# Performance work log

Hardware: AMD Instinct MI355X
Metric: run time of the kernel (lower is better)

The kernel has to match this reference:

```python
import jax, jax.numpy as jnp
import numpy as np

NUM_HEADS = 16
HEAD_DIM = 64
ROPE_BASE = 160000.0


def _rope_tables(seq_len, head_dim):
    inv_freq = 1.0 / (ROPE_BASE ** (jnp.arange(0, head_dim, 2, dtype=jnp.float32) / head_dim))
    freqs = jnp.arange(seq_len, dtype=jnp.float32)[:, None] * inv_freq[None, :]  # [S, hd/2]
    return jnp.cos(freqs)[None, None], jnp.sin(freqs)[None, None]  # [1,1,S,hd/2]


def _apply_rope(x, cos, sin):
    # x: [B, nh, S, hd]; split-half rotation as in the torch module
    x1, x2 = jnp.split(x, 2, axis=-1)
    return jnp.concatenate([x1 * cos - x2 * sin, x2 * cos + x1 * sin], axis=-1)


def setup_inputs() -> dict:
    key = jax.random.key(0)
    k1, k2, k3 = jax.random.split(key, 3)
    B, S, H = 2, 2048, 1024
    hidden_states = jax.random.normal(k1, (B, S, H), dtype=jnp.float32)
    # additive causal mask: 0 for allowed, -1e9 for future positions
    causal = jnp.tril(jnp.ones((S, S), dtype=bool))
    attention_mask = jnp.where(causal, 0.0, -1e9).astype(jnp.float32)[None, None]
    Wqkv = jax.random.normal(k2, (H, 3 * H), dtype=jnp.float32) * (H ** -0.5)
    Wo = jax.random.normal(k3, (H, H), dtype=jnp.float32) * (H ** -0.5)
    return {"hidden_states": hidden_states, "attention_mask": attention_mask, "Wqkv": Wqkv, "Wo": Wo}


def reference(hidden_states, attention_mask, Wqkv, Wo):
    B, S, H = hidden_states.shape
    nh, hd = NUM_HEADS, HEAD_DIM
    scale = hd ** -0.5

    qkv = hidden_states @ Wqkv                                   # [B,S,3H]
    qkv = qkv.reshape(B, S, 3, nh, hd).transpose(2, 0, 3, 1, 4)  # [3,B,nh,S,hd]
    q, k, v = qkv[0], qkv[1], qkv[2]

    cos, sin = _rope_tables(S, hd)
    q = _apply_rope(q, cos, sin)
    k = _apply_rope(k, cos, sin)

    scores = jnp.einsum('bhqd,bhkd->bhqk', q, k) * scale + attention_mask
    attn = jax.nn.softmax(scores, axis=-1)
    out = jnp.einsum('bhqk,bhkd->bhqd', attn, v)                 # [B,nh,S,hd]
    out = out.transpose(0, 2, 1, 3).reshape(B, S, H)
    return out @ Wo
```

## Files before the change

### kernel.cpp

```cpp
#include <hip/hip_runtime.h>
#include <hip/hip_bf16.h>

typedef __bf16 bf16x8 __attribute__((ext_vector_type(8)));
typedef float f32x4 __attribute__((ext_vector_type(4)));
typedef unsigned short u16;

__device__ __forceinline__ u16 f2bf(float f) {
    union { float f; unsigned u; } x{f};
    unsigned r = x.u + 0x7fffu + ((x.u >> 16) & 1u);
    return (u16)(r >> 16);
}
__device__ __forceinline__ unsigned pk2(float a, float b) {
    union { float f; unsigned u; } x{a}, y{b};
    return ((x.u + 0x8000u) >> 16) | ((y.u + 0x8000u) & 0xffff0000u);
}
__device__ __forceinline__ float ex2(float x) { return __builtin_amdgcn_exp2f(x); }
__device__ __forceinline__ f32x4 zero4() { f32x4 z = {0.f, 0.f, 0.f, 0.f}; return z; }

typedef const __attribute__((address_space(1))) unsigned int* gp1_t;
typedef __attribute__((address_space(3))) unsigned int* lp3_t;
__device__ __forceinline__ void async16(const u16* g, u16* l) {
    __builtin_amdgcn_global_load_lds((gp1_t)g, (lp3_t)l, 16, 0, 0);
}

__global__ void __launch_bounds__(256) prep(const float* __restrict__ hs,
                                            u16* __restrict__ Xb,
                                            const float* __restrict__ Wqkv,
                                            u16* __restrict__ Wqkvt,
                                            const float* __restrict__ Wo,
                                            u16* __restrict__ Wot,
                                            float* __restrict__ cosT,
                                            float* __restrict__ sinT) {
    __shared__ float tile[32][33];
    const int blk = blockIdx.x, t = threadIdx.x;
    if (blk < 4096) {
        int i = (blk * 256 + t) * 4;
        float4 v = *(const float4*)(hs + i);
        ushort4 o;
        o.x = f2bf(v.x); o.y = f2bf(v.y); o.z = f2bf(v.z); o.w = f2bf(v.w);
        *(ushort4*)(Xb + i) = o;
    } else if (blk < 8192) {
        const float* W; u16* Wt; int N, bx, by;
        if (blk < 7168) { int bid = blk - 4096; W = Wqkv; Wt = Wqkvt; N = 3072; bx = bid % 96; by = bid / 96; }
        else            { int bid = blk - 7168; W = Wo;   Wt = Wot;   N = 1024; bx = bid % 32; by = bid / 32; }
        const int K = 1024;
        int tx = t & 31, ty = t >> 5;
        int n0 = bx * 32, k0 = by * 32;
#pragma unroll
        for (int i = 0; i < 32; i += 8)
            tile[ty + i][tx] = W[(size_t)(k0 + ty + i) * N + n0 + tx];
        __syncthreads();
#pragma unroll
        for (int i = 0; i < 32; i += 8)
            Wt[(size_t)(n0 + ty + i) * K + k0 + tx] = f2bf(tile[tx][ty + i]);
    } else {
        int idx = (blk - 8192) * 256 + t;
        int d = idx & 31, s = idx >> 5;
        float inv = expf(-(float)d * 0.374466538f);
        float th = (float)s * inv;
        cosT[idx] = cosf(th);
        sinT[idx] = sinf(th);
    }
}

struct GemmCtx {
    f32x4 acc[4][4];
    int m16, q4, wm, wn;
};
template <int KDIM>
__device__ __forceinline__ void gemm_loop(const u16* __restrict__ A,
                                          const u16* __restrict__ Bt,
                                          int bm, int bn, GemmCtx& cx,
                                          u16* As, u16* Bs) {
    const int t = threadIdx.x;
    const int lane = t & 63, w = t >> 6;
    cx.wm = w >> 1; cx.wn = w & 1;
    cx.m16 = lane & 15; cx.q4 = lane >> 4;

    const int lrow = lane >> 2;
    const int kchunk = (lane & 3) ^ ((lane >> 3) & 3);
    const u16* Ag = A + (size_t)(bm * 128 + w * 32 + lrow) * KDIM + kchunk * 8;
    const u16* Bg = Bt + (size_t)(bn * 128 + w * 32 + lrow) * KDIM + kchunk * 8;
    const int l0 = (w * 32) * 32;
    const int l1 = (w * 32 + 16) * 32;
    const int kswz = (cx.q4 ^ ((cx.m16 >> 1) & 3)) * 8;

#pragma unroll
    for (int i = 0; i < 4; i++)
#pragma unroll
        for (int j = 0; j < 4; j++) cx.acc[i][j] = zero4();

    constexpr int NT = KDIM / 32;
    async16(Ag, As + l0);
    async16(Ag + 16 * KDIM, As + l1);
    async16(Bg, Bs + l0);
    async16(Bg + 16 * KDIM, Bs + l1);
    async16(Ag + 32, As + 4096 + l0);
    async16(Ag + 16 * KDIM + 32, As + 4096 + l1);
    async16(Bg + 32, Bs + 4096 + l0);
    async16(Bg + 16 * KDIM + 32, Bs + 4096 + l1);

    int co = 0, po = 2 * 4096;
#pragma unroll 1
    for (int tt = 0; tt < NT; ++tt) {
        if (tt + 1 < NT) {
            asm volatile("s_waitcnt vmcnt(4)" ::: "memory");
        } else {
            asm volatile("s_waitcnt vmcnt(0)" ::: "memory");
        }
        __builtin_amdgcn_s_barrier();
        __builtin_amdgcn_sched_barrier(0);
        if (tt + 2 < NT) {
            const int k0 = (tt + 2) * 32;
            async16(Ag + k0, As + po + l0);
            async16(Ag + 16 * KDIM + k0, As + po + l1);
            async16(Bg + k0, Bs + po + l0);
            async16(Bg + 16 * KDIM + k0, Bs + po + l1);
        }
        __builtin_amdgcn_sched_barrier(0);

        bf16x8 af[4], bf[4];
#pragma unroll
        for (int i = 0; i < 4; i++)
            af[i] = *(const bf16x8*)&As[co + (cx.wm * 64 + i * 16 + cx.m16) * 32 + kswz];
#pragma unroll
        for (int j = 0; j < 4; j++)
            bf[j] = *(const bf16x8*)&Bs[co + (cx.wn * 64 + j * 16 + cx.m16) * 32 + kswz];
#pragma unroll
        for (int i = 0; i < 4; i++)
#pragma unroll
            for (int j = 0; j < 4; j++)
                cx.acc[i][j] = __builtin_amdgcn_mfma_f32_16x16x32_bf16(af[i], bf[j], cx.acc[i][j], 0, 0, 0);

        asm volatile("" ::: "memory");
        __builtin_amdgcn_sched_barrier(0);
        co += 4096; if (co == 12288) co = 0;
        po += 4096; if (po == 12288) po = 0;
    }
}

struct GemmCtx2 {
    f32x4 acc[4][8];
    int m16, q4, wm;
};
template <int KDIM>
__device__ __forceinline__ void gemm_loop2(const u16* __restrict__ A,
                                           const u16* __restrict__ Bt,
                                           int bm, int bn, GemmCtx2& cx,
                                           u16* As, u16* Bs) {
    const int t = threadIdx.x;
    const int lane = t & 63, w = t >> 6;
    cx.wm = w;
    cx.m16 = lane & 15; cx.q4 = lane >> 4;

    const int lrow = lane >> 2;
    const int kchunk = (lane & 3) ^ ((lane >> 3) & 3);
    const u16* Ag = A + (size_t)(bm * 128 + w * 64 + lrow) * KDIM + kchunk * 8;
    const u16* Bg = Bt + (size_t)(bn * 128 + w * 64 + lrow) * KDIM + kchunk * 8;
    const int lb = (w * 64) * 32;
    const int kswz = (cx.q4 ^ ((cx.m16 >> 1) & 3)) * 8;

#pragma unroll
    for (int i = 0; i < 4; i++)
#pragma unroll
        for (int j = 0; j < 8; j++) cx.acc[i][j] = zero4();

    constexpr int NT = KDIM / 32;
#pragma unroll
    for (int c = 0; c < 4; c++) {
        async16(Ag + c * 16 * KDIM, As + lb + c * 16 * 32);
        async16(Bg + c * 16 * KDIM, Bs + lb + c * 16 * 32);
    }
#pragma unroll
    for (int c = 0; c < 4; c++) {
        async16(Ag + 32 + c * 16 * KDIM, As + 4096 + lb + c * 16 * 32);
        async16(Bg + 32 + c * 16 * KDIM, Bs + 4096 + lb + c * 16 * 32);
    }

    int co = 0, po = 2 * 4096;
#pragma unroll 1
    for (int tt = 0; tt < NT; ++tt) {
        if (tt + 1 < NT) {
            asm volatile("s_waitcnt vmcnt(8)" ::: "memory");
        } else {
            asm volatile("s_waitcnt vmcnt(0)" ::: "memory");
        }
        __builtin_amdgcn_s_barrier();
        __builtin_amdgcn_sched_barrier(0);
        if (tt + 2 < NT) {
            const int k0 = (tt + 2) * 32;
#pragma unroll
            for (int c = 0; c < 4; c++) {
                async16(Ag + k0 + c * 16 * KDIM, As + po + lb + c * 16 * 32);
                async16(Bg + k0 + c * 16 * KDIM, Bs + po + lb + c * 16 * 32);
            }
        }
        __builtin_amdgcn_sched_barrier(0);

        bf16x8 af[4], bf[8];
#pragma unroll
        for (int i = 0; i < 4; i++)
            af[i] = *(const bf16x8*)&As[co + (cx.wm * 64 + i * 16 + cx.m16) * 32 + kswz];
#pragma unroll
        for (int j = 0; j < 8; j++)
            bf[j] = *(const bf16x8*)&Bs[co + (j * 16 + cx.m16) * 32 + kswz];
#pragma unroll
        for (int i = 0; i < 4; i++)
#pragma unroll
            for (int j = 0; j < 8; j++)
                cx.acc[i][j] = __builtin_amdgcn_mfma_f32_16x16x32_bf16(af[i], bf[j], cx.acc[i][j], 0, 0, 0);

        asm volatile("" ::: "memory");
        __builtin_amdgcn_sched_barrier(0);
        co += 4096; if (co == 12288) co = 0;
        po += 4096; if (po == 12288) po = 0;
    }
}

__global__ void __launch_bounds__(128, 2) gemm_qkv(const u16* __restrict__ A,
                                                   const u16* __restrict__ Bt,
                                                   const float* __restrict__ cosT,
                                                   const float* __restrict__ sinT,
                                                   u16* __restrict__ Q,
                                                   u16* __restrict__ Kd,
                                                   u16* __restrict__ Vt) {
    __shared__ __align__(16) u16 As[3 * 128 * 32];
    __shared__ __align__(16) u16 Bs[3 * 128 * 32];
    GemmCtx2 cx;
    const int hw = blockIdx.x;
    const int orig = (hw & 7) * 96 + (hw >> 3);
    const int bm = orig / 24, bn = orig % 24;
    gemm_loop2<1024>(A, Bt, bm, bn, cx, As, Bs);
    const int m16 = cx.m16, q4 = cx.q4;

    const int colblk = bn * 128;
    const int type = colblk >> 10;
    const int h0 = (colblk & 1023) >> 6;
    const int rbase = bm * 128 + cx.wm * 64;

    if (type == 2) {
#pragma unroll
        for (int i = 0; i < 4; i++) {
            int s0 = rbase + i * 16 + q4 * 4;
            int b = s0 >> 11, sl = s0 & 2047;
#pragma unroll
            for (int j = 0; j < 8; j++) {
                int h = h0 + (j >> 2);
                int d = (j & 3) * 16 + m16;
                size_t ob = (size_t)(b * 16 + h) * 64 * 2048;
                ushort4 o;
                o.x = f2bf(cx.acc[i][j][0]);
                o.y = f2bf(cx.acc[i][j][1]);
                o.z = f2bf(cx.acc[i][j][2]);
                o.w = f2bf(cx.acc[i][j][3]);
                *(ushort4*)&Vt[ob + (size_t)d * 2048 + sl] = o;
            }
        }
    } else {
        u16* dst = (type == 0) ? Q : Kd;
        const float qs = (type == 0) ? 0.1803368801f  : 1.0f;
#pragma unroll
        for (int i = 0; i < 4; i++)
#pragma unroll
            for (int rr = 0; rr < 4; rr++) {
                int r = rbase + i * 16 + q4 * 4 + rr;
                int b = r >> 11, s = r & 2047;
#pragma unroll
                for (int hh = 0; hh < 2; hh++) {
                    size_t ob = ((size_t)((b * 16 + h0 + hh) * 2048 + s)) * 64;
#pragma unroll
                    for (int j2 = 0; j2 < 2; j2++) {
                        int d = j2 * 16 + m16;
                        float cs = cosT[s * 32 + d];
                        float sn = sinT[s * 32 + d];
                        float x1 = cx.acc[i][hh * 4 + j2][rr];
                        float x2 = cx.acc[i][hh * 4 + j2 + 2][rr];
                        dst[ob + d]      = f2bf((x1 * cs - x2 * sn) * qs);
                        dst[ob + d + 32] = f2bf((x2 * cs + x1 * sn) * qs);
                    }
                }
            }
    }
}

__global__ void __launch_bounds__(256) gemm_out(const u16* __restrict__ A,
                                                const u16* __restrict__ Bt,
                                                float* __restrict__ C) {
    __shared__ __align__(16) u16 As[3 * 128 * 32];
    __shared__ __align__(16) u16 Bs[3 * 128 * 32];
    GemmCtx cx;
    const int bm = blockIdx.y, bn = blockIdx.x;
    gemm_loop<1024>(A, Bt, bm, bn, cx, As, Bs);
    const int N = 1024;
#pragma unroll
    for (int i = 0; i < 4; i++)
#pragma unroll
        for (int j = 0; j < 4; j++)
#pragma unroll
            for (int rr = 0; rr < 4; rr++) {
                int row = bm * 128 + cx.wm * 64 + i * 16 + cx.q4 * 4 + rr;
                int col = bn * 128 + cx.wn * 64 + j * 16 + cx.m16;
                C[(size_t)row * N + col] = cx.acc[i][j][rr];
            }
}

__global__ void __launch_bounds__(512) attn_kernel(const u16* __restrict__ Q,
                                                   const u16* __restrict__ Kg_,
                                                   const u16* __restrict__ Vtg_,
                                                   u16* __restrict__ O) {
    __shared__ __align__(16) u16 Ks[2][64][72];
    __shared__ __align__(16) u16 Vs[2][64][72];
    __shared__ __align__(16) u16 Pt[8][16][72];
    const int t = threadIdx.x, w = t >> 6;
    const int m16 = t & 15, q4 = (t & 63) >> 4;
    const int bx = blockIdx.x, bh = blockIdx.y;
    const size_t base = (size_t)bh * 2048 * 64;
    const int b = bh >> 4, h = bh & 15;
    const int skey = t >> 3, sc = (t & 7) * 8;

#pragma unroll 1
    for (int ph = 0; ph < 2; ph++) {
        const int st = ph ? (15 - bx) : bx;
        const int qrow = st * 128 + w * 16 + m16;
        const u16* Qg = Q + base + (size_t)qrow * 64;
        bf16x8 qf0 = *(const bf16x8*)(Qg + q4 * 8);
        bf16x8 qf1 = *(const bf16x8*)(Qg + 32 + q4 * 8);

        f32x4 occ[4];
#pragma unroll
        for (int dc = 0; dc < 4; dc++) occ[dc] = zero4();
        float li = 0.f;

        const int jtmax = 2 * st + 1;
        const int jd = 2 * st + (w >> 2);

        const u16* Kb0 = Kg_ + base + skey * 64 + sc;
        const u16* Vt0 = Vtg_ + base + (size_t)skey * 2048 + sc;
        uint4 ka = *(const uint4*)(Kb0);
        uint4 va = *(const uint4*)(Vt0);

#pragma unroll 1
        for (int jt = 0; jt <= jtmax; jt++) {
            const int bi = jt & 1;
            *(uint4*)&Ks[bi][skey][sc] = ka;
            *(uint4*)&Vs[bi][skey][sc] = va;
            if (jt < jtmax) {
                ka = *(const uint4*)(Kb0 + (size_t)(jt + 1) * 4096);
                va = *(const uint4*)(Vt0 + (size_t)(jt + 1) * 64);
            }
            __syncthreads();

            if (jt <= jd) {
                f32x4 stv[4];
#pragma unroll
                for (int c = 0; c < 4; c++) stv[c] = zero4();
#pragma unroll
                for (int c = 0; c < 4; c++) {
                    bf16x8 kf0 = *(const bf16x8*)&Ks[bi][c * 16 + m16][q4 * 8];
                    bf16x8 kf1 = *(const bf16x8*)&Ks[bi][c * 16 + m16][32 + q4 * 8];
                    stv[c] = __builtin_amdgcn_mfma_f32_16x16x32_bf16(kf0, qf0, stv[c], 0, 0, 0);
                    stv[c] = __builtin_amdgcn_mfma_f32_16x16x32_bf16(kf1, qf1, stv[c], 0, 0, 0);
                }

                float pv[4][4];
#pragma unroll
                for (int c = 0; c < 4; c++)
#pragma unroll
                    for (int rr = 0; rr < 4; rr++) pv[c][rr] = stv[c][rr];
                if (jt == jd) {
                    const int ql = qrow - 64 * jt;
#pragma unroll
                    for (int c = 0; c < 4; c++)
#pragma unroll
                        for (int rr = 0; rr < 4; rr++)
                            if (c * 16 + q4 * 4 + rr > ql) pv[c][rr] = -1e30f;
                }

#pragma unroll
                for (int c = 0; c < 4; c++) {
                    float p0 = ex2(pv[c][0] - 24.f);
                    float p1 = ex2(pv[c][1] - 24.f);
                    float p2 = ex2(pv[c][2] - 24.f);
                    float p3 = ex2(pv[c][3] - 24.f);
                    li += (p0 + p1) + (p2 + p3);
                    *(uint2*)&Pt[w][m16][c * 16 + q4 * 4] = make_uint2(pk2(p0, p1), pk2(p2, p3));
                }

#pragma unroll
                for (int ks = 0; ks < 2; ks++) {
                    bf16x8 pf = *(const bf16x8*)&Pt[w][m16][ks * 32 + q4 * 8];
#pragma unroll
                    for (int dc = 0; dc < 4; dc++) {
                        bf16x8 vf = *(const bf16x8*)&Vs[bi][dc * 16 + m16][ks * 32 + q4 * 8];
                        occ[dc] = __builtin_amdgcn_mfma_f32_16x16x32_bf16(vf, pf, occ[dc], 0, 0, 0);
                    }
                }
            }
        }

        li += __shfl_xor(li, 16);
        li += __shfl_xor(li, 32);
        float rli = 1.0f / li;
        u16* Op = O + ((size_t)(b * 2048 + qrow)) * 1024 + h * 64 + q4 * 4;
#pragma unroll
        for (int dc = 0; dc < 4; dc++) {
            ushort4 o;
            o.x = f2bf(occ[dc][0] * rli);
            o.y = f2bf(occ[dc][1] * rli);
            o.z = f2bf(occ[dc][2] * rli);
            o.w = f2bf(occ[dc][3] * rli);
            *(ushort4*)(Op + dc * 16) = o;
        }
        __syncthreads();
    }
}

extern "C" void kernel_launch(void* const* d_in, const int* in_sizes, int n_in,
                              void* d_out, int out_size, void* d_ws, size_t ws_size,
                              hipStream_t stream) {
    const float* hs   = (const float*)d_in[0];
    const float* Wqkv = (const float*)d_in[2];
    const float* Wo   = (const float*)d_in[3];
    float* out = (float*)d_out;

    const int BS = 4096;
    const int H = 1024, N3 = 3072;
    const int SH = 32 * 2048 * 64;

    u16* Xb    = (u16*)d_ws;
    u16* Wqkvt = Xb + (size_t)BS * H;
    u16* Wot   = Wqkvt + (size_t)N3 * H;
    u16* Qb    = Wot + (size_t)H * H;
    u16* Kb    = Qb + SH;
    u16* Vtb   = Kb + SH;
    u16* AOb   = Vtb + SH;
    float* cosT = (float*)(AOb + (size_t)BS * H);
    float* sinT = cosT + 2048 * 32;

    prep<<<8448, 256, 0, stream>>>(hs, Xb, Wqkv, Wqkvt, Wo, Wot, cosT, sinT);

    gemm_qkv<<<768, 128, 0, stream>>>(Xb, Wqkvt, cosT, sinT, Qb, Kb, Vtb);

    attn_kernel<<<dim3(8, 32), 512, 0, stream>>>(Qb, Kb, Vtb, AOb);

    gemm_out<<<dim3(H / 128, BS / 128), 256, 0, stream>>>(AOb, Wot, out);
}
```

Measured before the change: 190.6 us.

## Enlarge QKV GEMM tiles to 256x256 with 512 threads and BK=64 double buffering

Rewrites the QKV projection GEMM to use 256x256 output tiles per block with 8 waves (2x4 wave grid, each wave 128x64), a K-step of 64 and double-buffered LDS, replacing 128x128 tiles with 2 waves and triple buffering at K=32. Larger tiles are meant to raise arithmetic intensity and cut global and LDS traffic per MFMA, and the epilogue is simplified to one head per wave. The costs are only 192 blocks on a GPU with about 256 CUs, so some CUs sit idle, plus heavier register pressure (32 accumulators per wave) and 128KB of LDS per block, which may block two blocks from sharing a CU. An extra barrier per iteration is also added.

```diff
diff --git a/kernel.cpp b/kernel.cpp
--- a/kernel.cpp
+++ b/kernel.cpp
@@ -139,115 +139,113 @@
     }
 }
 
-struct GemmCtx2 {
-    f32x4 acc[4][8];
-    int m16, q4, wm;
+struct GemmCtx3 {
+    f32x4 acc[8][4];
+    int m16, q4, wm, wn;
 };
 template <int KDIM>
-__device__ __forceinline__ void gemm_loop2(const u16* __restrict__ A,
+__device__ __forceinline__ void gemm_loop3(const u16* __restrict__ A,
                                            const u16* __restrict__ Bt,
-                                           int bm, int bn, GemmCtx2& cx,
+                                           int bm, int bn, GemmCtx3& cx,
                                            u16* As, u16* Bs) {
     const int t = threadIdx.x;
     const int lane = t & 63, w = t >> 6;
-    cx.wm = w;
+    cx.wm = w >> 2; cx.wn = w & 3;
     cx.m16 = lane & 15; cx.q4 = lane >> 4;
 
-    const int lrow = lane >> 2;
-    const int kchunk = (lane & 3) ^ ((lane >> 3) & 3);
-    const u16* Ag = A + (size_t)(bm * 128 + w * 64 + lrow) * KDIM + kchunk * 8;
-    const u16* Bg = Bt + (size_t)(bn * 128 + w * 64 + lrow) * KDIM + kchunk * 8;
-    const int lb = (w * 64) * 32;
-    const int kswz = (cx.q4 ^ ((cx.m16 >> 1) & 3)) * 8;
-
-#pragma unroll
-    for (int i = 0; i < 4; i++)
-#pragma unroll
-        for (int j = 0; j < 8; j++) cx.acc[i][j] = zero4();
-
-    constexpr int NT = KDIM / 32;
+    const int srow = lane >> 3;
+    const int schunk = (lane & 7) ^ (srow & 7);
+    const u16* Ag = A + (size_t)(bm * 256 + w * 32 + srow) * KDIM + schunk * 8;
+    const u16* Bg = Bt + (size_t)(bn * 256 + w * 32 + srow) * KDIM + schunk * 8;
+    const int lb = (w * 32) * 64;
+
+#pragma unroll
+    for (int i = 0; i < 8; i++)
+#pragma unroll
+        for (int j = 0; j < 4; j++) cx.acc[i][j] = zero4();
+
+    constexpr int NT = KDIM / 64;
+    constexpr int HB = 256 * 64;
+
 #pragma unroll
     for (int c = 0; c < 4; c++) {
-        async16(Ag + c * 16 * KDIM, As + lb + c * 16 * 32);
-        async16(Bg + c * 16 * KDIM, Bs + lb + c * 16 * 32);
-    }
-#pragma unroll
-    for (int c = 0; c < 4; c++) {
-        async16(Ag + 32 + c * 16 * KDIM, As + 4096 + lb + c * 16 * 32);
-        async16(Bg + 32 + c * 16 * KDIM, Bs + 4096 + lb + c * 16 * 32);
-    }
-
-    int co = 0, po = 2 * 4096;
+        async16(Ag + c * 8 * KDIM, As + lb + c * 8 * 64);
+        async16(Bg + c * 8 * KDIM, Bs + lb + c * 8 * 64);
+    }
+
 #pragma unroll 1
     for (int tt = 0; tt < NT; ++tt) {
+        const int co = (tt & 1) * HB;
         if (tt + 1 < NT) {
+            const int no = HB - co;
+            const int k0 = (tt + 1) * 64;
+#pragma unroll
+            for (int c = 0; c < 4; c++) {
+                async16(Ag + k0 + c * 8 * KDIM, As + no + lb + c * 8 * 64);
+                async16(Bg + k0 + c * 8 * KDIM, Bs + no + lb + c * 8 * 64);
+            }
             asm volatile("s_waitcnt vmcnt(8)" ::: "memory");
         } else {
             asm volatile("s_waitcnt vmcnt(0)" ::: "memory");
         }
         __builtin_amdgcn_s_barrier();
-        __builtin_amdgcn_sched_barrier(0);
-        if (tt + 2 < NT) {
-            const int k0 = (tt + 2) * 32;
-#pragma unroll
-            for (int c = 0; c < 4; c++) {
-                async16(Ag + k0 + c * 16 * KDIM, As + po + lb + c * 16 * 32);
-                async16(Bg + k0 + c * 16 * KDIM, Bs + po + lb + c * 16 * 32);
-            }
-        }
-        __builtin_amdgcn_sched_barrier(0);
-
-        bf16x8 af[4], bf[8];
-#pragma unroll
-        for (int i = 0; i < 4; i++)
-            af[i] = *(const bf16x8*)&As[co + (cx.wm * 64 + i * 16 + cx.m16) * 32 + kswz];
-#pragma unroll
-        for (int j = 0; j < 8; j++)
-            bf[j] = *(const bf16x8*)&Bs[co + (j * 16 + cx.m16) * 32 + kswz];
-#pragma unroll
-        for (int i = 0; i < 4; i++)
-#pragma unroll
-            for (int j = 0; j < 8; j++)
-                cx.acc[i][j] = __builtin_amdgcn_mfma_f32_16x16x32_bf16(af[i], bf[j], cx.acc[i][j], 0, 0, 0);
-
         asm volatile("" ::: "memory");
         __builtin_amdgcn_sched_barrier(0);
-        co += 4096; if (co == 12288) co = 0;
-        po += 4096; if (po == 12288) po = 0;
-    }
-}
-
-__global__ void __launch_bounds__(128, 2) gemm_qkv(const u16* __restrict__ A,
+
+        const int m7 = cx.m16 & 7;
+#pragma unroll
+        for (int ks = 0; ks < 2; ks++) {
+            const int slot = ((ks * 4 + cx.q4) ^ m7) * 8;
+            bf16x8 af[8], bf[4];
+#pragma unroll
+            for (int i = 0; i < 8; i++)
+                af[i] = *(const bf16x8*)&As[co + (cx.wm * 128 + i * 16 + cx.m16) * 64 + slot];
+#pragma unroll
+            for (int j = 0; j < 4; j++)
+                bf[j] = *(const bf16x8*)&Bs[co + (cx.wn * 64 + j * 16 + cx.m16) * 64 + slot];
+#pragma unroll
+            for (int i = 0; i < 8; i++)
+#pragma unroll
+                for (int j = 0; j < 4; j++)
+                    cx.acc[i][j] = __builtin_amdgcn_mfma_f32_16x16x32_bf16(af[i], bf[j], cx.acc[i][j], 0, 0, 0);
+        }
+
+        asm volatile("" ::: "memory");
+        __builtin_amdgcn_sched_barrier(0);
+        __builtin_amdgcn_s_barrier();
+    }
+}
+
+__global__ void __launch_bounds__(512, 2) gemm_qkv(const u16* __restrict__ A,
                                                    const u16* __restrict__ Bt,
                                                    const float* __restrict__ cosT,
                                                    const float* __restrict__ sinT,
                                                    u16* __restrict__ Q,
                                                    u16* __restrict__ Kd,
                                                    u16* __restrict__ Vt) {
-    __shared__ __align__(16) u16 As[3 * 128 * 32];
-    __shared__ __align__(16) u16 Bs[3 * 128 * 32];
-    GemmCtx2 cx;
+    __shared__ __align__(16) u16 As[2 * 256 * 64];
+    __shared__ __align__(16) u16 Bs[2 * 256 * 64];
+    GemmCtx3 cx;
     const int hw = blockIdx.x;
-    const int orig = (hw & 7) * 96 + (hw >> 3);
-    const int bm = orig / 24, bn = orig % 24;
-    gemm_loop2<1024>(A, Bt, bm, bn, cx, As, Bs);
+    const int orig = (hw & 7) * 24 + (hw >> 3);
+    const int bm = orig / 12, bn = orig % 12;
+    gemm_loop3<1024>(A, Bt, bm, bn, cx, As, Bs);
     const int m16 = cx.m16, q4 = cx.q4;
 
-    const int colblk = bn * 128;
-    const int type = colblk >> 10;
-    const int h0 = (colblk & 1023) >> 6;
-    const int rbase = bm * 128 + cx.wm * 64;
+    const int colbase = bn * 256 + cx.wn * 64;
+    const int type = colbase >> 10;
+    const int h = (colbase & 1023) >> 6;
+    const int rbase = bm * 256 + cx.wm * 128;
 
     if (type == 2) {
 #pragma unroll
-        for (int i = 0; i < 4; i++) {
+        for (int i = 0; i < 8; i++) {
             int s0 = rbase + i * 16 + q4 * 4;
             int b = s0 >> 11, sl = s0 & 2047;
-#pragma unroll
-            for (int j = 0; j < 8; j++) {
-                int h = h0 + (j >> 2);
-                int d = (j & 3) * 16 + m16;
-                size_t ob = (size_t)(b * 16 + h) * 64 * 2048;
+            size_t ob = (size_t)(b * 16 + h) * 64 * 2048;
+#pragma unroll
+            for (int j = 0; j < 4; j++) {
+                int d = j * 16 + m16;
                 ushort4 o;
                 o.x = f2bf(cx.acc[i][j][0]);
                 o.y = f2bf(cx.acc[i][j][1]);
@@ -260,24 +258,21 @@
         u16* dst = (type == 0) ? Q : Kd;
         const float qs = (type == 0) ? 0.1803368801f  : 1.0f;
 #pragma unroll
-        for (int i = 0; i < 4; i++)
+        for (int i = 0; i < 8; i++)
 #pragma unroll
             for (int rr = 0; rr < 4; rr++) {
                 int r = rbase + i * 16 + q4 * 4 + rr;
                 int b = r >> 11, s = r & 2047;
-#pragma unroll
-                for (int hh = 0; hh < 2; hh++) {
-                    size_t ob = ((size_t)((b * 16 + h0 + hh) * 2048 + s)) * 64;
-#pragma unroll
-                    for (int j2 = 0; j2 < 2; j2++) {
-                        int d = j2 * 16 + m16;
-                        float cs = cosT[s * 32 + d];
-                        float sn = sinT[s * 32 + d];
-                        float x1 = cx.acc[i][hh * 4 + j2][rr];
-                        float x2 = cx.acc[i][hh * 4 + j2 + 2][rr];
-                        dst[ob + d]      = f2bf((x1 * cs - x2 * sn) * qs);
-                        dst[ob + d + 32] = f2bf((x2 * cs + x1 * sn) * qs);
-                    }
+                size_t ob = ((size_t)((b * 16 + h) * 2048 + s)) * 64;
+#pragma unroll
+                for (int j2 = 0; j2 < 2; j2++) {
+                    int d = j2 * 16 + m16;
+                    float cs = cosT[s * 32 + d];
+                    float sn = sinT[s * 32 + d];
+                    float x1 = cx.acc[i][j2][rr];
+                    float x2 = cx.acc[i][j2 + 2][rr];
+                    dst[ob + d]      = f2bf((x1 * cs - x2 * sn) * qs);
+                    dst[ob + d + 32] = f2bf((x2 * cs + x1 * sn) * qs);
                 }
             }
     }
@@ -439,7 +434,7 @@
 
     prep<<<8448, 256, 0, stream>>>(hs, Xb, Wqkv, Wqkvt, Wo, Wot, cosT, sinT);
 
-    gemm_qkv<<<768, 128, 0, stream>>>(Xb, Wqkvt, cosT, sinT, Qb, Kb, Vtb);
+    gemm_qkv<<<192, 512, 0, stream>>>(Xb, Wqkvt, cosT, sinT, Qb, Kb, Vtb);
 
     attn_kernel<<<dim3(8, 32), 512, 0, stream>>>(Qb, Kb, Vtb, AOb);
 
```

Result: no change. 191.8 us (+0.6%).
